# Performance work log

Measured on AMD Instinct MI355X. Metric: run time of the kernel, lower is better.

Reference implementation:

```python
import jax, jax.numpy as jnp
import numpy as np

LN_EPS = 1e-5  # torch F.layer_norm default

def _layer_norm(c):
    mu = jnp.mean(c, axis=-1, keepdims=True)
    var = jnp.mean((c - mu) ** 2, axis=-1, keepdims=True)
    return (c - mu) * jax.lax.rsqrt(var + LN_EPS)

def _ln_lstm_cell(x, h, c, wx, wh, b):
    # wx: (4, H, in)  used as x @ wx[g].T ; wh: (4, H, H) used as h @ wh[g] (NO transpose,
    # matching the original torch code which only transposes the input weight).
    # gate order: i, f, o, c_tilde
    pre = jnp.einsum('bi,ghi->gbh', x, wx) + jnp.einsum('bh,ghk->gbk', h, wh) + b[:, None, :]
    i = jax.nn.sigmoid(pre[0])
    f = jax.nn.sigmoid(pre[1])
    o = jax.nn.sigmoid(pre[2])
    c_tilde = jnp.tanh(pre[3])
    c_new = _layer_norm(f * c + i * c_tilde)
    h_new = o * jnp.tanh(c_new)
    return h_new, c_new

def setup_inputs() -> dict:
    key = jax.random.key(0)
    ks = jax.random.split(key, 8)
    BS, SEQ, OBS, H, LOGIT = 512, 64, 512, 1024, 1024
    w = lambda k, *s: jax.random.normal(k, s, jnp.float32) * 0.02
    return {
        'obs': jax.random.normal(ks[0], (BS, SEQ, OBS), jnp.float32),
        'fc1_w': w(ks[1], H, OBS),
        'fc1_b': jnp.zeros((H,), jnp.float32),
        'wx1': w(ks[2], 4, H, H),
        'wh1': w(ks[3], 4, H, H),
        'b1': jnp.zeros((4, H), jnp.float32),
        'wx2': w(ks[4], 4, H, H),
        'wh2': w(ks[5], 4, H, H),
        'b2': jnp.zeros((4, H), jnp.float32),
        'fc2_w': w(ks[6], LOGIT, H),
        'fc2_b': jnp.zeros((LOGIT,), jnp.float32),
    }

def reference(obs, fc1_w, fc1_b, wx1, wh1, b1, wx2, wh2, b2, fc2_w, fc2_b):
    # obs: (bs, seq, obs_shape)
    x = jnp.einsum('bso,ho->bsh', obs, fc1_w) + fc1_b  # fc1 over all timesteps
    bs, seq, H = x.shape
    z = jnp.zeros((bs, H), x.dtype)

    def step(carry, xt):
        h0, c0, h1, c1 = carry
        h0, c0 = _ln_lstm_cell(xt, h0, c0, wx1, wh1, b1)  # layer 1
        h1, c1 = _ln_lstm_cell(h0, h1, c1, wx2, wh2, b2)  # layer 2 (dropout = identity in eval)
        return (h0, c0, h1, c1), None

    (h0, c0, h1, c1), _ = jax.lax.scan(step, (z, z, z, z), jnp.swapaxes(x, 0, 1))
    logit = h1 @ fc2_w.T + fc2_b
    h_n = jnp.stack((h0, h1), axis=0)
    c_n = jnp.stack((c0, c1), axis=0)
    return logit, h_n, c_n
```

## Files before the change

### kernel.cpp

```cpp
#include <hip/hip_runtime.h>
#include <hip/hip_bf16.h>
#include <hip/hip_fp16.h>

using half_t = _Float16;
typedef __attribute__((ext_vector_type(8))) _Float16 f16x8;
typedef __attribute__((ext_vector_type(4))) _Float16 f16x4;
typedef __attribute__((ext_vector_type(4))) float f32x4;

#define LN_EPS 1e-5f

__device__ inline void gll16(const void* g, void* ldsbase) {
    __builtin_amdgcn_global_load_lds(
        (const __attribute__((address_space(1))) void*)g,
        (__attribute__((address_space(3))) void*)ldsbase, 16, 0, 0);
}

__device__ inline float block_sum(float v, float* sred) {
    #pragma unroll
    for (int off = 32; off; off >>= 1) v += __shfl_down(v, off, 64);
    __syncthreads();
    if ((threadIdx.x & 63) == 0) sred[threadIdx.x >> 6] = v;
    __syncthreads();
    return sred[0] + sred[1] + sred[2] + sred[3];
}

__device__ inline void cell_block(
    int b, const half_t* __restrict__ preA, const half_t* __restrict__ preB,
    const float* __restrict__ bias,
    float* __restrict__ cst, half_t* __restrict__ hs,
    float* __restrict__ hf, bool final_step)
{
    __shared__ float sred[4];
    const int t = threadIdx.x;
    const int hi = t * 4;
    const size_t pb = (size_t)b * 4096 + hi;
    const size_t cb = (size_t)b * 1024 + hi;

    float pre[4][4];
    #pragma unroll
    for (int g = 0; g < 4; ++g) {
        f16x4 a4 = *(const f16x4*)&preA[pb + g*1024];
        f16x4 v4 = *(const f16x4*)&preB[pb + g*1024];
        float4 bs = *(const float4*)&bias[g*1024 + hi];
        pre[g][0] = (float)a4[0] + (float)v4[0] + bs.x;
        pre[g][1] = (float)a4[1] + (float)v4[1] + bs.y;
        pre[g][2] = (float)a4[2] + (float)v4[2] + bs.z;
        pre[g][3] = (float)a4[3] + (float)v4[3] + bs.w;
    }
    float4 c4 = *(const float4*)&cst[cb];
    float co[4] = {c4.x, c4.y, c4.z, c4.w};

    float cn[4], og[4], s = 0.f;
    #pragma unroll
    for (int j = 0; j < 4; ++j) {
        float ig = 1.f / (1.f + expf(-pre[0][j]));
        float fg = 1.f / (1.f + expf(-pre[1][j]));
        og[j]    = 1.f / (1.f + expf(-pre[2][j]));
        float ct = tanhf(pre[3][j]);
        cn[j] = fg * co[j] + ig * ct;
        s += cn[j];
    }
    float mu  = block_sum(s, sred) * (1.f/1024.f);
    float vs = 0.f;
    #pragma unroll
    for (int j = 0; j < 4; ++j) { float d = cn[j] - mu; vs += d*d; }
    float var = block_sum(vs, sred) * (1.f/1024.f);
    float rs  = rsqrtf(var + LN_EPS);

    float4 cw, hw; f16x4 h16w;
    #pragma unroll
    for (int j = 0; j < 4; ++j) {
        float cv = (cn[j] - mu) * rs;
        float hv = og[j] * tanhf(cv);
        ((float*)&cw)[j] = cv;
        ((float*)&hw)[j] = hv;
        h16w[j] = (half_t)hv;
    }
    *(float4*)&cst[cb] = cw;
    *(f16x4*)&hs[cb]   = h16w;
    if (final_step) *(float4*)&hf[cb] = hw;
}

__global__ __launch_bounds__(256) void cells_kernel(
    const half_t* __restrict__ preA1, const half_t* __restrict__ preB1,
    const half_t* __restrict__ preA2, const half_t* __restrict__ preB2,
    const float* __restrict__ b1x, const float* __restrict__ b2,
    float* __restrict__ c0, float* __restrict__ c1,
    half_t* __restrict__ h0s, half_t* __restrict__ h1s,
    float* __restrict__ h0f, float* __restrict__ h1f, int st)
{
    const int blk = blockIdx.x;
    if (blk < 512) {
        cell_block(blk, preA1, preB1, b1x, c0, h0s, h0f, st == 63);
    } else {
        if (st == 0) return;
        cell_block(blk - 512, preA2, preB2, b2, c1, h1s, h1f, false);
    }
}

__global__ __launch_bounds__(256) void cells_final(
    const half_t* __restrict__ preA2, const half_t* __restrict__ preB2,
    const float* __restrict__ b2,
    float* __restrict__ c1, half_t* __restrict__ h1s, float* __restrict__ h1f)
{
    cell_block(blockIdx.x, preA2, preB2, b2, c1, h1s, h1f, true);
}

__global__ __launch_bounds__(256, 2) void step_gemm4(
    const half_t* __restrict__ obs16,
    const half_t* __restrict__ W1x, const half_t* __restrict__ wx2c,
    const half_t* __restrict__ wh1t, const half_t* __restrict__ wh2t,
    half_t* __restrict__ preA1, half_t* __restrict__ preA2,
    half_t* __restrict__ preB1, half_t* __restrict__ preB2,
    const half_t* __restrict__ h0s, const half_t* __restrict__ h1s, int st)
{
    __shared__ __align__(16) unsigned char sA[2][16384];
    __shared__ __align__(16) unsigned char sB[2][16384];

    const int wg = blockIdx.x;
    const int ylo = wg & 7;
    int r = wg >> 3;
    const int x = r & 3; r >>= 2;
    const int z = r & 3; r >>= 2;
    const int y = ylo + 8 * r;

    if (z == 3 && st == 63) return;

    const half_t* A; const half_t* B; half_t* C; size_t lda, ldb; int nkt;
    if (z == 0)      { A = h0s; lda = 1024; B = wx2c; ldb = 1024; C = preA2; nkt = 16; }
    else if (z == 1) { A = h1s; lda = 1024; B = wh2t; ldb = 1024; C = preB2; nkt = 16; }
    else if (z == 2) { A = h0s; lda = 1024; B = wh1t; ldb = 1024; C = preB1; nkt = 16; }
    else { A = obs16 + (size_t)(st+1) * 512; lda = 32768; B = W1x; ldb = 512; C = preA1; nkt = 8; }

    const int t = threadIdx.x, l = t & 63, w = t >> 6;
    const int wr = (w >> 1) * 64, wc = (w & 1) * 64;
    const int rowbase = x * 128, colbase = y * 128;

    int srow[4], sch[4];
    #pragma unroll
    for (int i = 0; i < 4; ++i) {
        int s = (w*4 + i)*64 + l;
        srow[i] = s >> 3;
        sch[i]  = ((s & 7) ^ (srow[i] & 7)) * 8;
    }

    f32x4 acc[4][4];
    #pragma unroll
    for (int m = 0; m < 4; ++m)
        #pragma unroll
        for (int n = 0; n < 4; ++n) acc[m][n] = (f32x4)(0.f);

    auto stage = [&](int kt, int buf) {
        const int ko = kt * 64;
        #pragma unroll
        for (int i = 0; i < 4; ++i) {
            gll16(A + (size_t)(rowbase+srow[i])*lda + ko + sch[i], &sA[buf][(w*4+i)*1024]);
            gll16(B + (size_t)(colbase+srow[i])*ldb + ko + sch[i], &sB[buf][(w*4+i)*1024]);
        }
    };

    stage(0, 0);
    for (int kt = 0; kt < nkt; ++kt) {
        const int buf = kt & 1;
        __syncthreads();
        if (kt + 1 < nkt) stage(kt + 1, buf ^ 1);
        #pragma unroll
        for (int kk = 0; kk < 2; ++kk) {
            const int chunk = kk*4 + (l >> 4);
            f16x8 bfr[4];
            #pragma unroll
            for (int n = 0; n < 4; ++n) {
                int rowb = wc + n*16 + (l & 15);
                bfr[n] = *(const f16x8*)&sB[buf][rowb*128 + ((chunk ^ (rowb & 7)) << 4)];
            }
            #pragma unroll
            for (int m = 0; m < 4; ++m) {
                int rowa = wr + m*16 + (l & 15);
                f16x8 af = *(const f16x8*)&sA[buf][rowa*128 + ((chunk ^ (rowa & 7)) << 4)];
                #pragma unroll
                for (int n = 0; n < 4; ++n)
                    acc[m][n] = __builtin_amdgcn_mfma_f32_16x16x32_f16(af, bfr[n], acc[m][n], 0, 0, 0);
            }
        }
    }

    #pragma unroll
    for (int m = 0; m < 4; ++m) {
        int row0 = rowbase + wr + m*16 + (l >> 4)*4;
        #pragma unroll
        for (int n = 0; n < 4; ++n) {
            int col = colbase + wc + n*16 + (l & 15);
            #pragma unroll
            for (int r2 = 0; r2 < 4; ++r2)
                C[(size_t)(row0+r2)*4096 + col] = (half_t)acc[m][n][r2];
        }
    }
}

struct GArgs {
    const half_t* A; const half_t* B; const float* bias; void* C;
    int lda, ldb, K, ldc, outhalf;
};

__global__ __launch_bounds__(256) void gemm_ms(GArgs g0, GArgs g1, GArgs g2,
                                               int gx, int gy, int gz, int rowpin)
{
    const int d = blockIdx.x;
    int x, y, z;
    if (rowpin) {
        const int xlo = d & 7;
        int r = d >> 3;
        y = r % gy;  r /= gy;
        z = r % gz;
        x = xlo + 8 * (r / gz);
    } else {
        const int ylo = d & 7;
        int r = d >> 3;
        x = r % gx;  r /= gx;
        z = r % gz;
        y = ylo + 8 * (r / gz);
    }

    const GArgs g = (z == 0) ? g0 : (z == 1 ? g1 : g2);

    __shared__ __align__(16) unsigned char sA[2][16384];
    __shared__ __align__(16) unsigned char sB[2][16384];

    const int t  = threadIdx.x;
    const int l  = t & 63;
    const int w  = t >> 6;
    const int wr = (w >> 1) * 64;
    const int wc = (w & 1)  * 64;
    const int rowbase = x * 128;
    const int colbase = y * 128;

    f32x4 acc[4][4];
    #pragma unroll
    for (int m = 0; m < 4; ++m)
        #pragma unroll
        for (int n = 0; n < 4; ++n) acc[m][n] = (f32x4)(0.f);

    int srow[4], sch[4];
    #pragma unroll
    for (int i = 0; i < 4; ++i) {
        int s = (w*4 + i)*64 + l;
        srow[i] = s >> 3;
        sch[i]  = ((s & 7) ^ (srow[i] & 7)) * 8;
    }

    const int nkt = g.K >> 6;

    auto stage = [&](int kt, int buf) {
        const int ko = kt * 64;
        #pragma unroll
        for (int i = 0; i < 4; ++i) {
            gll16(g.A + (size_t)(rowbase+srow[i])*g.lda + ko + sch[i], &sA[buf][(w*4+i)*1024]);
            gll16(g.B + (size_t)(colbase+srow[i])*g.ldb + ko + sch[i], &sB[buf][(w*4+i)*1024]);
        }
    };

    stage(0, 0);
    for (int kt = 0; kt < nkt; ++kt) {
        const int buf = kt & 1;
        __syncthreads();
        if (kt + 1 < nkt) stage(kt + 1, buf ^ 1);
        #pragma unroll
        for (int kk = 0; kk < 2; ++kk) {
            const int chunk = kk*4 + (l >> 4);
            f16x8 bfr[4];
            #pragma unroll
            for (int n = 0; n < 4; ++n) {
                int rowb = wc + n*16 + (l & 15);
                bfr[n] = *(const f16x8*)&sB[buf][rowb*128 + ((chunk ^ (rowb & 7)) << 4)];
            }
            #pragma unroll
            for (int m = 0; m < 4; ++m) {
                int rowa = wr + m*16 + (l & 15);
                f16x8 af = *(const f16x8*)&sA[buf][rowa*128 + ((chunk ^ (rowa & 7)) << 4)];
                #pragma unroll
                for (int n = 0; n < 4; ++n)
                    acc[m][n] = __builtin_amdgcn_mfma_f32_16x16x32_f16(af, bfr[n], acc[m][n], 0, 0, 0);
            }
        }
    }

    #pragma unroll
    for (int m = 0; m < 4; ++m) {
        int row0 = rowbase + wr + m*16 + (l >> 4)*4;
        #pragma unroll
        for (int n = 0; n < 4; ++n) {
            int col = colbase + wc + n*16 + (l & 15);
            float bv = g.bias ? g.bias[col] : 0.f;
            #pragma unroll
            for (int r2 = 0; r2 < 4; ++r2) {
                float v = acc[m][n][r2] + bv;
                if (g.outhalf) ((half_t*)g.C)[(size_t)(row0+r2)*g.ldc + col] = (half_t)v;
                else           ((float*)g.C)[(size_t)(row0+r2)*g.ldc + col] = v;
            }
        }
    }
}

__global__ __launch_bounds__(256) void transpose_wh_cvt(
    const float* __restrict__ wh1, const float* __restrict__ wh2,
    half_t* __restrict__ o1, half_t* __restrict__ o2)
{
    __shared__ float tile[64][65];
    const int z = blockIdx.z;
    const float* src = (z < 4 ? wh1 : wh2) + (size_t)(z & 3) * 1024 * 1024;
    half_t*      dst = (z < 4 ? o1  : o2 ) + (size_t)(z & 3) * 1024 * 1024;
    const int kb = blockIdx.x * 64, nb = blockIdx.y * 64;
    const int t = threadIdx.x;
    #pragma unroll
    for (int i = 0; i < 16; ++i) {
        int idx = t + i*256, r = idx >> 6, c = idx & 63;
        tile[r][c] = src[(size_t)(kb + r)*1024 + nb + c];
    }
    __syncthreads();
    #pragma unroll
    for (int i = 0; i < 16; ++i) {
        int idx = t + i*256, r = idx >> 6, c = idx & 63;
        dst[(size_t)(nb + r)*1024 + kb + c] = (half_t)tile[c][r];
    }
}

__global__ __launch_bounds__(256) void transpose_fc1(
    const float* __restrict__ fc1_w, half_t* __restrict__ fc1t)
{
    __shared__ float tile[64][65];
    const int hb = blockIdx.x * 64, ob = blockIdx.y * 64;
    const int t = threadIdx.x;
    #pragma unroll
    for (int i = 0; i < 16; ++i) {
        int idx = t + i*256, r = idx >> 6, c = idx & 63;
        tile[r][c] = fc1_w[(size_t)(hb + r)*512 + ob + c];
    }
    __syncthreads();
    #pragma unroll
    for (int i = 0; i < 16; ++i) {
        int idx = t + i*256, r = idx >> 6, c = idx & 63;
        fc1t[(size_t)(ob + r)*1024 + hb + c] = (half_t)tile[c][r];
    }
}

__global__ __launch_bounds__(256) void fold_b1(
    const float* __restrict__ wx1, const float* __restrict__ fc1_b,
    const float* __restrict__ b1, float* __restrict__ b1x)
{
    __shared__ float sred[4];
    const int j = blockIdx.x, t = threadIdx.x;
    float4 wv = *(const float4*)&wx1[(size_t)j*1024 + t*4];
    float4 bv = *(const float4*)&fc1_b[t*4];
    float s = wv.x*bv.x + wv.y*bv.y + wv.z*bv.z + wv.w*bv.w;
    float tot = block_sum(s, sred);
    if (t == 0) b1x[j] = b1[j] + tot;
}

__global__ __launch_bounds__(256) void cvt_f32_f16(
    const float* __restrict__ in, half_t* __restrict__ out, int n8)
{
    int i = blockIdx.x * 256 + threadIdx.x;
    if (i >= n8) return;
    float4 lo = ((const float4*)in)[2*i];
    float4 hi = ((const float4*)in)[2*i + 1];
    union { uint4 v; half_t h[8]; } r;
    r.h[0]=(half_t)lo.x; r.h[1]=(half_t)lo.y; r.h[2]=(half_t)lo.z; r.h[3]=(half_t)lo.w;
    r.h[4]=(half_t)hi.x; r.h[5]=(half_t)hi.y; r.h[6]=(half_t)hi.z; r.h[7]=(half_t)hi.w;
    ((uint4*)out)[i] = r.v;
}

__global__ __launch_bounds__(256) void pack_out(
    const float* __restrict__ h0, const float* __restrict__ h1,
    const float* __restrict__ c0, const float* __restrict__ c1, float* __restrict__ out)
{
    const int NSZ = 512 * 1024;
    int i = blockIdx.x * 256 + threadIdx.x;
    out[NSZ     + i] = h0[i];
    out[2*NSZ   + i] = h1[i];
    out[3*NSZ   + i] = c0[i];
    out[4*NSZ   + i] = c1[i];
}

extern "C" void kernel_launch(void* const* d_in, const int* in_sizes, int n_in,
                              void* d_out, int out_size, void* d_ws, size_t ws_size,
                              hipStream_t stream)
{
    const float* obs   = (const float*)d_in[0];
    const float* fc1_w = (const float*)d_in[1];
    const float* fc1_b = (const float*)d_in[2];
    const float* wx1   = (const float*)d_in[3];
    const float* wh1   = (const float*)d_in[4];
    const float* b1    = (const float*)d_in[5];
    const float* wx2   = (const float*)d_in[6];
    const float* wh2   = (const float*)d_in[7];
    const float* b2    = (const float*)d_in[8];
    const float* fc2_w = (const float*)d_in[9];
    const float* fc2_b = (const float*)d_in[10];
    float* out = (float*)d_out;

    char* ws = (char*)d_ws;
    size_t off = 0;
    auto carve = [&](size_t bytes) -> char* {
        char* p = ws + off; off += (bytes + 255) & ~(size_t)255; return p;
    };
    half_t* obs16 = (half_t*)carve((size_t)512*64*512*2);
    half_t* wx1c  = (half_t*)carve((size_t)4096*1024*2);
    half_t* wh1t  = (half_t*)carve((size_t)4096*1024*2);
    half_t* wx2c  = (half_t*)carve((size_t)4096*1024*2);
    half_t* wh2t  = (half_t*)carve((size_t)4096*1024*2);
    half_t* fc1t  = (half_t*)carve((size_t)512*1024*2);
    half_t* W1x   = (half_t*)carve((size_t)4096*512*2);
    half_t* fc2c  = (half_t*)carve((size_t)1024*1024*2);
    float*  b1x   = (float*) carve((size_t)4096*4);
    half_t* preA1 = (half_t*)carve((size_t)512*4096*2);
    half_t* preA2 = (half_t*)carve((size_t)512*4096*2);
    half_t* preB1 = (half_t*)carve((size_t)512*4096*2);
    half_t* preB2 = (half_t*)carve((size_t)512*4096*2);
    half_t* h0s   = (half_t*)carve((size_t)512*1024*2);
    half_t* h1s   = (half_t*)carve((size_t)512*1024*2);
    float*  h0f   = (float*) carve((size_t)512*1024*4);
    float*  h1f   = (float*) carve((size_t)512*1024*4);
    float*  c0    = (float*) carve((size_t)512*1024*4);
    float*  c1    = (float*) carve((size_t)512*1024*4);

    hipMemsetAsync(h1s, 0, (size_t)512*1024*2, stream);
    hipMemsetAsync(c0,  0, (size_t)512*1024*4, stream);
    hipMemsetAsync(c1,  0, (size_t)512*1024*4, stream);
    hipMemsetAsync(preB1, 0, (size_t)512*4096*2, stream);

    cvt_f32_f16<<<8192, 256, 0, stream>>>(obs,   obs16, 512*64*512/8);
    cvt_f32_f16<<<2048, 256, 0, stream>>>(wx1,   wx1c,  4*1024*1024/8);
    cvt_f32_f16<<<2048, 256, 0, stream>>>(wx2,   wx2c,  4*1024*1024/8);
    cvt_f32_f16<<<512,  256, 0, stream>>>(fc2_w, fc2c,  1024*1024/8);
    transpose_wh_cvt<<<dim3(16,16,8), 256, 0, stream>>>(wh1, wh2, wh1t, wh2t);
    transpose_fc1<<<dim3(16,8), 256, 0, stream>>>(fc1_w, fc1t);
    fold_b1<<<4096, 256, 0, stream>>>(wx1, fc1_b, b1, b1x);

    GArgs Z{};
    auto ga = [](const half_t* A, int lda, const half_t* B, int ldb, int K,
                 const float* bias, void* C, int ldc, int outhalf) {
        GArgs g; g.A=A; g.B=B; g.bias=bias; g.C=C;
        g.lda=lda; g.ldb=ldb; g.K=K; g.ldc=ldc; g.outhalf=outhalf; return g;
    };

    gemm_ms<<<128, 256, 0, stream>>>(
        ga(wx1c, 1024, fc1t, 1024, 1024, nullptr, W1x, 512, 1), Z, Z, 32, 4, 1, 1);
    gemm_ms<<<128, 256, 0, stream>>>(
        ga(obs16, 32768, W1x, 512, 512, nullptr, preA1, 4096, 1), Z, Z, 4, 32, 1, 0);

    for (int st = 0; st < 64; ++st) {
        cells_kernel<<<1024, 256, 0, stream>>>(
            preA1, preB1, preA2, preB2, b1x, b2,
            c0, c1, h0s, h1s, h0f, h1f, st);
        step_gemm4<<<512, 256, 0, stream>>>(
            obs16, W1x, wx2c, wh1t, wh2t,
            preA1, preA2, preB1, preB2, h0s, h1s, st);
    }
    cells_final<<<512, 256, 0, stream>>>(preA2, preB2, b2, c1, h1s, h1f);

    gemm_ms<<<4*8, 256, 0, stream>>>(
        ga(h1s, 1024, fc2c, 1024, 1024, fc2_b, out, 1024, 0), Z, Z, 4, 8, 1, 0);
    pack_out<<<2048, 256, 0, stream>>>(h0f, h1f, c0, c1, out);
}
```

Measured before the change: 2.255 ms.

## Fuse obs fp32-to-fp16 conversion into step GEMM and write final states directly

Drops the upfront fp16 conversion of the whole observation tensor. The step GEMM's x-projection slice now loads fp32 observation rows into registers and converts them to fp16 before writing them into LDS. The initial x-projection uses the step GEMM with st=-1 in place of the generic GEMM. Final h/c states are written straight into the output buffer, which removes the pack_out kernel and its intermediate buffers. This costs extra fp32 bandwidth and register pressure on the z==3 tiles, plus a non-async load path that may stall the pipeline.

Result: faster. 2.039 ms (median of 2 runs) (-9.6%).

```diff
diff --git a/kernel.cpp b/kernel.cpp
--- a/kernel.cpp
+++ b/kernel.cpp
@@ -28,7 +28,7 @@
     int b, const half_t* __restrict__ preA, const half_t* __restrict__ preB,
     const float* __restrict__ bias,
     float* __restrict__ cst, half_t* __restrict__ hs,
-    float* __restrict__ hf, bool final_step)
+    float* __restrict__ hf, float* __restrict__ cf, bool final_step)
 {
     __shared__ float sred[4];
     const int t = threadIdx.x;
@@ -78,7 +78,10 @@
     }
     *(float4*)&cst[cb] = cw;
     *(f16x4*)&hs[cb]   = h16w;
-    if (final_step) *(float4*)&hf[cb] = hw;
+    if (final_step) {
+        *(float4*)&hf[cb] = hw;
+        *(float4*)&cf[cb] = cw;
+    }
 }
 
 __global__ __launch_bounds__(256) void cells_kernel(
@@ -87,27 +90,32 @@
     const float* __restrict__ b1x, const float* __restrict__ b2,
     float* __restrict__ c0, float* __restrict__ c1,
     half_t* __restrict__ h0s, half_t* __restrict__ h1s,
-    float* __restrict__ h0f, float* __restrict__ h1f, int st)
-{
+    float* __restrict__ out, int st)
+{
+    const int NSZ = 512 * 1024;
     const int blk = blockIdx.x;
     if (blk < 512) {
-        cell_block(blk, preA1, preB1, b1x, c0, h0s, h0f, st == 63);
+        cell_block(blk, preA1, preB1, b1x, c0, h0s,
+                   out + NSZ, out + 3*NSZ, st == 63);
     } else {
         if (st == 0) return;
-        cell_block(blk - 512, preA2, preB2, b2, c1, h1s, h1f, false);
+        cell_block(blk - 512, preA2, preB2, b2, c1, h1s,
+                   nullptr, nullptr, false);
     }
 }
 
 __global__ __launch_bounds__(256) void cells_final(
     const half_t* __restrict__ preA2, const half_t* __restrict__ preB2,
     const float* __restrict__ b2,
-    float* __restrict__ c1, half_t* __restrict__ h1s, float* __restrict__ h1f)
-{
-    cell_block(blockIdx.x, preA2, preB2, b2, c1, h1s, h1f, true);
+    float* __restrict__ c1, half_t* __restrict__ h1s, float* __restrict__ out)
+{
+    const int NSZ = 512 * 1024;
+    cell_block(blockIdx.x, preA2, preB2, b2, c1, h1s,
+               out + 2*NSZ, out + 4*NSZ, true);
 }
 
 __global__ __launch_bounds__(256, 2) void step_gemm4(
-    const half_t* __restrict__ obs16,
+    const float* __restrict__ obsF,
     const half_t* __restrict__ W1x, const half_t* __restrict__ wx2c,
     const half_t* __restrict__ wh1t, const half_t* __restrict__ wh2t,
     half_t* __restrict__ preA1, half_t* __restrict__ preA2,
@@ -124,13 +132,17 @@
     const int z = r & 3; r >>= 2;
     const int y = ylo + 8 * r;
 
-    if (z == 3 && st == 63) return;
+    const bool zx = (z == 3);
+    if (zx && st == 63) return;
+    if (st < 0 && !zx) return;
 
     const half_t* A; const half_t* B; half_t* C; size_t lda, ldb; int nkt;
+    const float* Af = nullptr;
     if (z == 0)      { A = h0s; lda = 1024; B = wx2c; ldb = 1024; C = preA2; nkt = 16; }
     else if (z == 1) { A = h1s; lda = 1024; B = wh2t; ldb = 1024; C = preB2; nkt = 16; }
     else if (z == 2) { A = h0s; lda = 1024; B = wh1t; ldb = 1024; C = preB1; nkt = 16; }
-    else { A = obs16 + (size_t)(st+1) * 512; lda = 32768; B = W1x; ldb = 512; C = preA1; nkt = 8; }
+    else { Af = obsF + (size_t)(st+1) * 512; A = nullptr; lda = 32768;
+           B = W1x; ldb = 512; C = preA1; nkt = 8; }
 
     const int t = threadIdx.x, l = t & 63, w = t >> 6;
     const int wr = (w >> 1) * 64, wc = (w & 1) * 64;
@@ -150,20 +162,53 @@
         #pragma unroll
         for (int n = 0; n < 4; ++n) acc[m][n] = (f32x4)(0.f);
 
-    auto stage = [&](int kt, int buf) {
+    float4 fv[8];
+    auto stageB = [&](int kt, int buf) {
         const int ko = kt * 64;
         #pragma unroll
+        for (int i = 0; i < 4; ++i)
+            gll16(B + (size_t)(colbase+srow[i])*ldb + ko + sch[i], &sB[buf][(w*4+i)*1024]);
+    };
+    auto stageA_h = [&](int kt, int buf) {
+        const int ko = kt * 64;
+        #pragma unroll
+        for (int i = 0; i < 4; ++i)
+            gll16(A + (size_t)(rowbase+srow[i])*lda + ko + sch[i], &sA[buf][(w*4+i)*1024]);
+    };
+    auto loadA_f = [&](int kt) {
+        const int ko = kt * 64;
+        #pragma unroll
         for (int i = 0; i < 4; ++i) {
-            gll16(A + (size_t)(rowbase+srow[i])*lda + ko + sch[i], &sA[buf][(w*4+i)*1024]);
-            gll16(B + (size_t)(colbase+srow[i])*ldb + ko + sch[i], &sB[buf][(w*4+i)*1024]);
-        }
-    };
-
-    stage(0, 0);
+            const float* p = Af + (size_t)(rowbase+srow[i])*lda + ko + sch[i];
+            fv[2*i]   = *(const float4*)p;
+            fv[2*i+1] = *(const float4*)(p + 4);
+        }
+    };
+    auto writeA_f = [&](int buf) {
+        #pragma unroll
+        for (int i = 0; i < 4; ++i) {
+            union { uint4 v; half_t h[8]; } rr;
+            rr.h[0]=(half_t)fv[2*i].x;   rr.h[1]=(half_t)fv[2*i].y;
+            rr.h[2]=(half_t)fv[2*i].z;   rr.h[3]=(half_t)fv[2*i].w;
+            rr.h[4]=(half_t)fv[2*i+1].x; rr.h[5]=(half_t)fv[2*i+1].y;
+            rr.h[6]=(half_t)fv[2*i+1].z; rr.h[7]=(half_t)fv[2*i+1].w;
+            *(uint4*)&sA[buf][((w*4+i)*64 + l)*16] = rr.v;
+        }
+    };
+
+    stageB(0, 0);
+    if (zx) { loadA_f(0); writeA_f(0); }
+    else    stageA_h(0, 0);
+
     for (int kt = 0; kt < nkt; ++kt) {
         const int buf = kt & 1;
         __syncthreads();
-        if (kt + 1 < nkt) stage(kt + 1, buf ^ 1);
+        const bool more = (kt + 1 < nkt);
+        if (more) {
+            stageB(kt + 1, buf ^ 1);
+            if (zx) loadA_f(kt + 1);
+            else    stageA_h(kt + 1, buf ^ 1);
+        }
         #pragma unroll
         for (int kk = 0; kk < 2; ++kk) {
             const int chunk = kk*4 + (l >> 4);
@@ -182,6 +227,7 @@
                     acc[m][n] = __builtin_amdgcn_mfma_f32_16x16x32_f16(af, bfr[n], acc[m][n], 0, 0, 0);
             }
         }
+        if (zx && more) writeA_f(buf ^ 1);
     }
 
     #pragma unroll
@@ -369,18 +415,6 @@
     ((uint4*)out)[i] = r.v;
 }
 
-__global__ __launch_bounds__(256) void pack_out(
-    const float* __restrict__ h0, const float* __restrict__ h1,
-    const float* __restrict__ c0, const float* __restrict__ c1, float* __restrict__ out)
-{
-    const int NSZ = 512 * 1024;
-    int i = blockIdx.x * 256 + threadIdx.x;
-    out[NSZ     + i] = h0[i];
-    out[2*NSZ   + i] = h1[i];
-    out[3*NSZ   + i] = c0[i];
-    out[4*NSZ   + i] = c1[i];
-}
-
 extern "C" void kernel_launch(void* const* d_in, const int* in_sizes, int n_in,
                               void* d_out, int out_size, void* d_ws, size_t ws_size,
                               hipStream_t stream)
@@ -403,7 +437,6 @@
     auto carve = [&](size_t bytes) -> char* {
         char* p = ws + off; off += (bytes + 255) & ~(size_t)255; return p;
     };
-    half_t* obs16 = (half_t*)carve((size_t)512*64*512*2);
     half_t* wx1c  = (half_t*)carve((size_t)4096*1024*2);
     half_t* wh1t  = (half_t*)carve((size_t)4096*1024*2);
     half_t* wx2c  = (half_t*)carve((size_t)4096*1024*2);
@@ -418,8 +451,6 @@
     half_t* preB2 = (half_t*)carve((size_t)512*4096*2);
     half_t* h0s   = (half_t*)carve((size_t)512*1024*2);
     half_t* h1s   = (half_t*)carve((size_t)512*1024*2);
-    float*  h0f   = (float*) carve((size_t)512*1024*4);
-    float*  h1f   = (float*) carve((size_t)512*1024*4);
     float*  c0    = (float*) carve((size_t)512*1024*4);
     float*  c1    = (float*) carve((size_t)512*1024*4);
 
@@ -428,7 +459,6 @@
     hipMemsetAsync(c1,  0, (size_t)512*1024*4, stream);
     hipMemsetAsync(preB1, 0, (size_t)512*4096*2, stream);
 
-    cvt_f32_f16<<<8192, 256, 0, stream>>>(obs,   obs16, 512*64*512/8);
     cvt_f32_f16<<<2048, 256, 0, stream>>>(wx1,   wx1c,  4*1024*1024/8);
     cvt_f32_f16<<<2048, 256, 0, stream>>>(wx2,   wx2c,  4*1024*1024/8);
     cvt_f32_f16<<<512,  256, 0, stream>>>(fc2_w, fc2c,  1024*1024/8);
@@ -445,20 +475,20 @@
 
     gemm_ms<<<128, 256, 0, stream>>>(
         ga(wx1c, 1024, fc1t, 1024, 1024, nullptr, W1x, 512, 1), Z, Z, 32, 4, 1, 1);
-    gemm_ms<<<128, 256, 0, stream>>>(
-        ga(obs16, 32768, W1x, 512, 512, nullptr, preA1, 4096, 1), Z, Z, 4, 32, 1, 0);
+    step_gemm4<<<512, 256, 0, stream>>>(
+        obs, W1x, wx2c, wh1t, wh2t,
+        preA1, preA2, preB1, preB2, h0s, h1s, -1);
 
     for (int st = 0; st < 64; ++st) {
         cells_kernel<<<1024, 256, 0, stream>>>(
             preA1, preB1, preA2, preB2, b1x, b2,
-            c0, c1, h0s, h1s, h0f, h1f, st);
+            c0, c1, h0s, h1s, out, st);
         step_gemm4<<<512, 256, 0, stream>>>(
-            obs16, W1x, wx2c, wh1t, wh2t,
+            obs, W1x, wx2c, wh1t, wh2t,
             preA1, preA2, preB1, preB2, h0s, h1s, st);
     }
-    cells_final<<<512, 256, 0, stream>>>(preA2, preB2, b2, c1, h1s, h1f);
+    cells_final<<<512, 256, 0, stream>>>(preA2, preB2, b2, c1, h1s, out);
 
     gemm_ms<<<4*8, 256, 0, stream>>>(
         ga(h1s, 1024, fc2c, 1024, 1024, fc2_b, out, 1024, 0), Z, Z, 4, 8, 1, 0);
-    pack_out<<<2048, 256, 0, stream>>>(h0f, h1f, c0, c1, out);
-}
+}
```
